# Kernel optimization log

Measured on AMD Instinct MI355X. Metric: run time of the kernel, lower is better.

The kernel has to match this reference:

```python
import jax, jax.numpy as jnp
import numpy as np

H = 2          # heads
C = 64         # hidden_dim per head
IN_DIM = 128
E_IN_DIM = 64
N_NODES = 50000
N_EDGES = 800000
NEG_SLOPE = 0.2


def gat_conv(x, edge_index, W, a_src, a_dst, bias):
    """PyG GATConv (heads=H, concat=False, add_self_loops=True).
    x: [N, F]; W: [F, H*C]; a_src/a_dst: [H, C]; bias: [C]."""
    N = x.shape[0]
    xw = (x @ W).reshape(N, H, C)                      # [N,H,C]
    loops = jnp.arange(N)
    src = jnp.concatenate([edge_index[0], loops])      # [E']
    dst = jnp.concatenate([edge_index[1], loops])
    a_s = jnp.einsum('nhc,hc->nh', xw, a_src)          # [N,H]
    a_d = jnp.einsum('nhc,hc->nh', xw, a_dst)
    e = jax.nn.leaky_relu(a_s[src] + a_d[dst], NEG_SLOPE)  # [E',H]
    # segment softmax over destination nodes (every node has a self-loop)
    m = jax.ops.segment_max(e, dst, num_segments=N)
    ex = jnp.exp(e - m[dst])
    den = jax.ops.segment_sum(ex, dst, num_segments=N)
    alpha = ex / den[dst]                              # [E',H]
    out = jax.ops.segment_sum(alpha[:, :, None] * xw[src], dst, num_segments=N)  # [N,H,C]
    return out.mean(axis=1) + bias                     # concat=False -> head mean


def setup_inputs() -> dict:
    key = jax.random.key(0)
    ks = jax.random.split(key, 16)
    s = 0.05
    return {
        'x': jax.random.normal(ks[0], (N_NODES, IN_DIM), jnp.float32),
        'xe': jax.random.normal(ks[1], (N_EDGES, E_IN_DIM), jnp.float32),
        'edge_index': jax.random.randint(ks[2], (2, N_EDGES), 0, N_NODES),
        # node GATConv params
        'Wn': jax.random.normal(ks[3], (IN_DIM, H * C), jnp.float32) * s,
        'asn': jax.random.normal(ks[4], (H, C), jnp.float32) * s,
        'adn': jax.random.normal(ks[5], (H, C), jnp.float32) * s,
        'bn': jnp.zeros((C,), jnp.float32),
        # edge GATConv params
        'We': jax.random.normal(ks[6], (E_IN_DIM, H * C), jnp.float32) * s,
        'ase': jax.random.normal(ks[7], (H, C), jnp.float32) * s,
        'ade': jax.random.normal(ks[8], (H, C), jnp.float32) * s,
        'be': jnp.zeros((C,), jnp.float32),
        # decoders
        'Wdx': jax.random.normal(ks[9], (C, IN_DIM), jnp.float32) * s,
        'bdx': jnp.zeros((IN_DIM,), jnp.float32),
        'Wde': jax.random.normal(ks[10], (C, E_IN_DIM), jnp.float32) * s,
        'bde': jnp.zeros((E_IN_DIM,), jnp.float32),
    }


def reference(x, xe, edge_index, Wn, asn, adn, bn, We, ase, ade, be, Wdx, bdx, Wde, bde):
    h_node = gat_conv(x, edge_index, Wn, asn, adn, bn)     # [N, C]
    h_edge = gat_conv(xe, edge_index, We, ase, ade, be)    # [E, C]
    x_rec = h_node @ Wdx + bdx                             # [N, in_dim]
    e_rec = h_edge @ Wde + bde                             # [E, edge_in_dim]
    return (x_rec, e_rec)
```

## Files before the change

### kernel.cpp

```cpp
#include <hip/hip_runtime.h>
#include <hip/hip_bf16.h>

constexpr int MAXD = 512;

__device__ __forceinline__ float lrelu(float v) { return v >= 0.f ? v : 0.2f * v; }

__global__ void count_kernel(const int* __restrict__ dst, int* __restrict__ cnt, int E) {
    int e = blockIdx.x * blockDim.x + threadIdx.x;
    if (e < E) atomicAdd(&cnt[dst[e]], 1);
}

__global__ __launch_bounds__(1024) void scan_kernel(const int* __restrict__ cnt, int* __restrict__ rowptr, int n) {
    __shared__ int part[1024];
    int t = threadIdx.x;
    int CH = (n + 1023) / 1024;
    int base = t * CH;
    int local = 0;
    for (int i = 0; i < CH; i++) { int idx = base + i; if (idx < n) local += cnt[idx]; }
    part[t] = local;
    __syncthreads();
    for (int o = 1; o < 1024; o <<= 1) {
        int v = (t >= o) ? part[t - o] : 0;
        __syncthreads();
        part[t] += v;
        __syncthreads();
    }
    int run = part[t] - local;
    for (int i = 0; i < CH; i++) {
        int idx = base + i;
        if (idx < n) { rowptr[idx] = run; run += cnt[idx]; }
    }
    if (t == 1023) rowptr[n] = run;
}

__global__ void scatter_kernel(const int* __restrict__ src, const int* __restrict__ dst,
                               int* __restrict__ cursor, int* __restrict__ ssrc, int E) {
    int e = blockIdx.x * blockDim.x + threadIdx.x;
    if (e < E) {
        int pos = atomicAdd(&cursor[dst[e]], 1);
        ssrc[pos] = src[e];
    }
}

__global__ void fold_kernel(const float* __restrict__ We, const float* __restrict__ Wde,
                            const float* __restrict__ be, const float* __restrict__ bde,
                            float* __restrict__ M, float* __restrict__ b0) {
    int j = threadIdx.x;
    int k = blockIdx.x;
    if (k < 64) {
        float s = 0.f;
        for (int c = 0; c < 64; c++)
            s = fmaf(0.5f * (We[k * 128 + c] + We[k * 128 + 64 + c]), Wde[c * 64 + j], s);
        M[k * 64 + j] = s;
    } else {
        float s = bde[j];
        for (int c = 0; c < 64; c++) s = fmaf(be[c], Wde[c * 64 + j], s);
        b0[j] = s;
    }
}

template <int K>
__global__ __launch_bounds__(256) void enc_gemm(const float* __restrict__ X, const float* __restrict__ W,
                                                const float* __restrict__ avs, const float* __restrict__ avd,
                                                float* __restrict__ xw, float* __restrict__ a_s,
                                                float* __restrict__ a_d, int Nn) {
    int n = blockIdx.x * 256 + threadIdx.x;
    int h = blockIdx.y;
    if (n >= Nn) return;
    const float* xr = X + (size_t)n * K;
    float acc[64];
#pragma unroll
    for (int j = 0; j < 64; j++) acc[j] = 0.f;
    for (int kc = 0; kc < K; kc += 16) {
        float xv[16];
#pragma unroll
        for (int i = 0; i < 16; i += 4) {
            float4 t = *(const float4*)(xr + kc + i);
            xv[i] = t.x; xv[i + 1] = t.y; xv[i + 2] = t.z; xv[i + 3] = t.w;
        }
#pragma unroll
        for (int k = 0; k < 16; k++) {
            const float* wr = W + (size_t)(kc + k) * 128 + h * 64;
#pragma unroll
            for (int j = 0; j < 64; j++) acc[j] = fmaf(xv[k], wr[j], acc[j]);
        }
    }
    float as = 0.f, ad = 0.f;
    const float* vs = avs + h * 64;
    const float* vd = avd + h * 64;
#pragma unroll
    for (int j = 0; j < 64; j++) { as = fmaf(acc[j], vs[j], as); ad = fmaf(acc[j], vd[j], ad); }
    float* xwr = xw + (size_t)n * 128 + h * 64;
#pragma unroll
    for (int j = 0; j < 64; j += 4) {
        float4 t = {acc[j], acc[j + 1], acc[j + 2], acc[j + 3]};
        *(float4*)(xwr + j) = t;
    }
    a_s[n * 2 + h] = as;
    a_d[n * 2 + h] = ad;
}

template <int OD>
__global__ __launch_bounds__(256) void rowmap_kernel(const float* __restrict__ A, const float* __restrict__ M,
                                                     const float* __restrict__ b0, float* __restrict__ out, int R) {
    __shared__ float4 sA4[128 * 16];
    __shared__ float4 sM4[64 * 16];
    int tid = threadIdx.x;
    int tr = tid & 15;
    int tj = tid >> 4;
    int jc = blockIdx.y * 64;
    int tile0 = blockIdx.x * 128;
    if (tile0 >= R) return;
    int nrows = min(128, R - tile0);

#pragma unroll
    for (int it = 0; it < 4; it++) {
        int f = tid + it * 256;
        int k = f >> 4, jq = f & 15;
        sM4[f] = *(const float4*)(M + (size_t)k * OD + jc + 4 * jq);
    }
    {
        const float4* Ag = (const float4*)(A + (size_t)tile0 * 64);
#pragma unroll
        for (int it = 0; it < 8; it++) {
            int e = tid + it * 256;
            int r = e >> 4, q = e & 15;
            int srcq = (r < nrows) ? e : q;
            sA4[(r << 4) | (q ^ (r & 15))] = Ag[srcq];
        }
    }
    __syncthreads();

    float4 b0v = *(const float4*)(b0 + jc + 4 * tj);
    float acc[8][4];
#pragma unroll
    for (int i = 0; i < 8; i++) { acc[i][0] = b0v.x; acc[i][1] = b0v.y; acc[i][2] = b0v.z; acc[i][3] = b0v.w; }

    for (int kq = 0; kq < 16; kq++) {
        float4 mf0 = sM4[(4 * kq + 0) * 16 + tj];
        float4 mf1 = sM4[(4 * kq + 1) * 16 + tj];
        float4 mf2 = sM4[(4 * kq + 2) * 16 + tj];
        float4 mf3 = sM4[(4 * kq + 3) * 16 + tj];
#pragma unroll
        for (int i = 0; i < 8; i++) {
            int row = tr + 16 * i;
            float4 af = sA4[(row << 4) | (kq ^ tr)];
            acc[i][0] = fmaf(af.x, mf0.x, acc[i][0]);
            acc[i][0] = fmaf(af.y, mf1.x, acc[i][0]);
            acc[i][0] = fmaf(af.z, mf2.x, acc[i][0]);
            acc[i][0] = fmaf(af.w, mf3.x, acc[i][0]);
            acc[i][1] = fmaf(af.x, mf0.y, acc[i][1]);
            acc[i][1] = fmaf(af.y, mf1.y, acc[i][1]);
            acc[i][1] = fmaf(af.z, mf2.y, acc[i][1]);
            acc[i][1] = fmaf(af.w, mf3.y, acc[i][1]);
            acc[i][2] = fmaf(af.x, mf0.z, acc[i][2]);
            acc[i][2] = fmaf(af.y, mf1.z, acc[i][2]);
            acc[i][2] = fmaf(af.z, mf2.z, acc[i][2]);
            acc[i][2] = fmaf(af.w, mf3.z, acc[i][2]);
            acc[i][3] = fmaf(af.x, mf0.w, acc[i][3]);
            acc[i][3] = fmaf(af.y, mf1.w, acc[i][3]);
            acc[i][3] = fmaf(af.z, mf2.w, acc[i][3]);
            acc[i][3] = fmaf(af.w, mf3.w, acc[i][3]);
        }
    }

#pragma unroll
    for (int i = 0; i < 8; i++) {
        int row = tr + 16 * i;
        if (row < nrows) {
            float4 t = {acc[i][0], acc[i][1], acc[i][2], acc[i][3]};
            *(float4*)(out + (size_t)(tile0 + row) * OD + jc + 4 * tj) = t;
        }
    }
}

__global__ __launch_bounds__(128) void msg_fused(
    const float* __restrict__ xw_n, const float* __restrict__ a_sn, const float* __restrict__ a_dn,
    const float* __restrict__ xw_e, const float* __restrict__ a_se, const float* __restrict__ a_de,
    const int* __restrict__ rowptr, const int* __restrict__ ssrc,
    const float* __restrict__ bn, const float* __restrict__ be,
    float* __restrict__ hm_n, float* __restrict__ hm_e) {
    int n = blockIdx.x;
    int tid = threadIdx.x;
    int h = tid >> 6, c = tid & 63;
    __shared__ int s_src[MAXD];
    __shared__ float t_n[2][MAXD];
    __shared__ float t_e[2][MAXD];
    __shared__ float red[8];
    __shared__ float hsh[2][128];

    int base = rowptr[n];
    int deg = rowptr[n + 1] - base;
    int degc = min(deg, MAXD);

    float adn0 = a_dn[n * 2 + 0], adn1 = a_dn[n * 2 + 1];
    float ade0 = a_de[n * 2 + 0], ade1 = a_de[n * 2 + 1];
    float2 asn_n = *(const float2*)(a_sn + (size_t)n * 2);
    float2 ase_n = *(const float2*)(a_se + (size_t)n * 2);
    float es_n0 = lrelu(asn_n.x + adn0), es_n1 = lrelu(asn_n.y + adn1);
    float es_e0 = lrelu(ase_n.x + ade0), es_e1 = lrelu(ase_n.y + ade1);

    for (int i = tid; i < degc; i += 128) {
        int s = ssrc[base + i];
        s_src[i] = s;
        float2 an = *(const float2*)(a_sn + (size_t)s * 2);
        float2 ae = *(const float2*)(a_se + (size_t)s * 2);
        t_n[0][i] = lrelu(an.x + adn0);
        t_n[1][i] = lrelu(an.y + adn1);
        t_e[0][i] = lrelu(ae.x + ade0);
        t_e[1][i] = lrelu(ae.y + ade1);
    }
    __syncthreads();

    int w = tid >> 6;
    int lane = tid & 63;
    {
        const float(*tt)[MAXD] = w ? t_e : t_n;
        const float* asx = w ? a_se : a_sn;
        float ad0 = w ? ade0 : adn0, ad1 = w ? ade1 : adn1;
        float es0 = w ? es_e0 : es_n0, es1 = w ? es_e1 : es_n1;
        float m0 = es0, m1 = es1;
        for (int i = lane; i < degc; i += 64) { m0 = fmaxf(m0, tt[0][i]); m1 = fmaxf(m1, tt[1][i]); }
        for (int i = MAXD + lane; i < deg; i += 64) {
            int s = ssrc[base + i];
            float2 a = *(const float2*)(asx + (size_t)s * 2);
            m0 = fmaxf(m0, lrelu(a.x + ad0)); m1 = fmaxf(m1, lrelu(a.y + ad1));
        }
#pragma unroll
        for (int o = 1; o < 64; o <<= 1) { m0 = fmaxf(m0, __shfl_xor(m0, o)); m1 = fmaxf(m1, __shfl_xor(m1, o)); }
        float d0 = 0.f, d1 = 0.f;
        for (int i = lane; i < degc; i += 64) { d0 += __expf(tt[0][i] - m0); d1 += __expf(tt[1][i] - m1); }
        for (int i = MAXD + lane; i < deg; i += 64) {
            int s = ssrc[base + i];
            float2 a = *(const float2*)(asx + (size_t)s * 2);
            d0 += __expf(lrelu(a.x + ad0) - m0); d1 += __expf(lrelu(a.y + ad1) - m1);
        }
#pragma unroll
        for (int o = 1; o < 64; o <<= 1) { d0 += __shfl_xor(d0, o); d1 += __shfl_xor(d1, o); }
        d0 += __expf(es0 - m0);
        d1 += __expf(es1 - m1);
        if (lane == 0) { red[w * 4 + 0] = m0; red[w * 4 + 1] = m1; red[w * 4 + 2] = d0; red[w * 4 + 3] = d1; }
    }
    __syncthreads();

    for (int i = tid; i < degc; i += 128) {
        t_n[0][i] = __expf(t_n[0][i] - red[0]);
        t_n[1][i] = __expf(t_n[1][i] - red[1]);
        t_e[0][i] = __expf(t_e[0][i] - red[4]);
        t_e[1][i] = __expf(t_e[1][i] - red[5]);
    }
    __syncthreads();

    float mn = red[h], dn_ = red[2 + h];
    float me = red[4 + h], de_ = red[6 + h];
    float accn = __expf((h ? es_n1 : es_n0) - mn) * xw_n[(size_t)n * 128 + h * 64 + c];
    float acce = __expf((h ? es_e1 : es_e0) - me) * xw_e[(size_t)n * 128 + h * 64 + c];
    for (int i = 0; i < degc; i++) {
        int s = s_src[i];
        float wn_ = t_n[h][i];
        float we_ = t_e[h][i];
        accn = fmaf(wn_, xw_n[(size_t)s * 128 + h * 64 + c], accn);
        acce = fmaf(we_, xw_e[(size_t)s * 128 + h * 64 + c], acce);
    }
    for (int i = MAXD; i < deg; i++) {
        int s = ssrc[base + i];
        float2 an = *(const float2*)(a_sn + (size_t)s * 2);
        float2 ae = *(const float2*)(a_se + (size_t)s * 2);
        float tn_ = lrelu(h ? (an.y + adn1) : (an.x + adn0));
        float te_ = lrelu(h ? (ae.y + ade1) : (ae.x + ade0));
        accn = fmaf(__expf(tn_ - mn), xw_n[(size_t)s * 128 + h * 64 + c], accn);
        acce = fmaf(__expf(te_ - me), xw_e[(size_t)s * 128 + h * 64 + c], acce);
    }
    hsh[0][tid] = accn / dn_;
    hsh[1][tid] = acce / de_;
    __syncthreads();
    if (tid < 64) {
        hm_n[(size_t)n * 64 + tid] = fmaf(0.5f, hsh[0][tid] + hsh[0][64 + tid], bn[tid]);
        hm_e[(size_t)n * 64 + tid] = fmaf(0.5f, hsh[1][tid] + hsh[1][64 + tid], be[tid]);
    }
}

extern "C" void kernel_launch(void* const* d_in, const int* in_sizes, int n_in,
                              void* d_out, int out_size, void* d_ws, size_t ws_size,
                              hipStream_t stream) {
    const float* x   = (const float*)d_in[0];
    const float* xe  = (const float*)d_in[1];
    const int*   ei  = (const int*)d_in[2];
    const float* Wn  = (const float*)d_in[3];
    const float* asn = (const float*)d_in[4];
    const float* adn = (const float*)d_in[5];
    const float* bn  = (const float*)d_in[6];
    const float* We  = (const float*)d_in[7];
    const float* ase = (const float*)d_in[8];
    const float* ade = (const float*)d_in[9];
    const float* be  = (const float*)d_in[10];
    const float* Wdx = (const float*)d_in[11];
    const float* bdx = (const float*)d_in[12];
    const float* Wde = (const float*)d_in[13];
    const float* bde = (const float*)d_in[14];

    const int N  = in_sizes[0] / 128;
    const int NE = in_sizes[1] / 64;
    const int E  = in_sizes[2] / 2;
    const int* src = ei;
    const int* dst = ei + E;

    char* wsb = (char*)d_ws;
    size_t off = 0;
    auto alloc = [&](size_t bytes) -> void* {
        void* p = wsb + off;
        off += (bytes + 255) & ~(size_t)255;
        return p;
    };
    float* xw_n = (float*)alloc((size_t)N * 128 * 4);
    float* a_sn = (float*)alloc((size_t)N * 2 * 4);
    float* a_dn = (float*)alloc((size_t)N * 2 * 4);
    float* xw_e = (float*)alloc((size_t)N * 128 * 4);
    float* a_se = (float*)alloc((size_t)N * 2 * 4);
    float* a_de = (float*)alloc((size_t)N * 2 * 4);
    float* hm_n = (float*)alloc((size_t)N * 64 * 4);
    float* hm_e = (float*)alloc((size_t)N * 64 * 4);
    float* Mt   = (float*)alloc((size_t)64 * 64 * 4);
    float* b0t  = (float*)alloc((size_t)64 * 4);
    int* cnt    = (int*)alloc((size_t)(N + 1) * 4);
    int* rowptr = (int*)alloc((size_t)(N + 1) * 4);
    int* cursor = (int*)alloc((size_t)(N + 1) * 4);
    int* ssrc   = (int*)alloc((size_t)E * 4);

    float* x_rec = (float*)d_out;
    float* e_rec = (float*)d_out + (size_t)N * 128;

    hipMemsetAsync(cnt, 0, (size_t)N * 4, stream);
    count_kernel<<<(E + 255) / 256, 256, 0, stream>>>(dst, cnt, E);
    scan_kernel<<<1, 1024, 0, stream>>>(cnt, rowptr, N);
    hipMemcpyAsync(cursor, rowptr, (size_t)N * 4, hipMemcpyDeviceToDevice, stream);
    scatter_kernel<<<(E + 255) / 256, 256, 0, stream>>>(src, dst, cursor, ssrc, E);

    fold_kernel<<<65, 64, 0, stream>>>(We, Wde, be, bde, Mt, b0t);

    enc_gemm<128><<<dim3((N + 255) / 256, 2), 256, 0, stream>>>(x, Wn, asn, adn, xw_n, a_sn, a_dn, N);
    enc_gemm<64><<<dim3((N + 255) / 256, 2), 256, 0, stream>>>(xe, We, ase, ade, xw_e, a_se, a_de, N);

    {
        int R = NE - N;
        rowmap_kernel<64><<<dim3((R + 127) / 128, 1), 256, 0, stream>>>(
            xe + (size_t)N * 64, Mt, b0t, e_rec + (size_t)N * 64, R);
    }

    msg_fused<<<N, 128, 0, stream>>>(xw_n, a_sn, a_dn, xw_e, a_se, a_de, rowptr, ssrc, bn, be, hm_n, hm_e);

    rowmap_kernel<128><<<dim3((N + 127) / 128, 2), 256, 0, stream>>>(hm_n, Wdx, bdx, x_rec, N);
    rowmap_kernel<64><<<dim3((N + 127) / 128, 1), 256, 0, stream>>>(hm_e, Wde, bde, e_rec, N);
}
```

Before: 846.9 us.

## Replace per-thread encoder GEMM with shared-memory tiled register-blocked GEMM

The node and edge encoder projections were computed one row per thread with 64 accumulators, reading W from global memory per FMA. They now use a 128x64 block tile staged in LDS with XOR-swizzled rows and 8x4 register blocking per thread. The attention-score dot products are reduced through shared memory. This cuts redundant global weight loads and register pressure, at the cost of extra LDS traffic and synchronisation.

```diff
diff --git a/kernel.cpp b/kernel.cpp
--- a/kernel.cpp
+++ b/kernel.cpp
@@ -60,44 +60,99 @@
 }
 
 template <int K>
-__global__ __launch_bounds__(256) void enc_gemm(const float* __restrict__ X, const float* __restrict__ W,
-                                                const float* __restrict__ avs, const float* __restrict__ avd,
-                                                float* __restrict__ xw, float* __restrict__ a_s,
-                                                float* __restrict__ a_d, int Nn) {
-    int n = blockIdx.x * 256 + threadIdx.x;
+__global__ __launch_bounds__(256) void enc_tiled(const float* __restrict__ X, const float* __restrict__ W,
+                                                 const float* __restrict__ avs, const float* __restrict__ avd,
+                                                 float* __restrict__ xw, float* __restrict__ a_s,
+                                                 float* __restrict__ a_d, int Nn) {
+    __shared__ float4 sA4[128 * 16];
+    __shared__ float4 sM4[64 * 16];
+    int tid = threadIdx.x;
+    int tr = tid & 15;
+    int tj = tid >> 4;
     int h = blockIdx.y;
-    if (n >= Nn) return;
-    const float* xr = X + (size_t)n * K;
-    float acc[64];
-#pragma unroll
-    for (int j = 0; j < 64; j++) acc[j] = 0.f;
-    for (int kc = 0; kc < K; kc += 16) {
-        float xv[16];
-#pragma unroll
-        for (int i = 0; i < 16; i += 4) {
-            float4 t = *(const float4*)(xr + kc + i);
-            xv[i] = t.x; xv[i + 1] = t.y; xv[i + 2] = t.z; xv[i + 3] = t.w;
-        }
-#pragma unroll
-        for (int k = 0; k < 16; k++) {
-            const float* wr = W + (size_t)(kc + k) * 128 + h * 64;
-#pragma unroll
-            for (int j = 0; j < 64; j++) acc[j] = fmaf(xv[k], wr[j], acc[j]);
-        }
-    }
-    float as = 0.f, ad = 0.f;
-    const float* vs = avs + h * 64;
-    const float* vd = avd + h * 64;
-#pragma unroll
-    for (int j = 0; j < 64; j++) { as = fmaf(acc[j], vs[j], as); ad = fmaf(acc[j], vd[j], ad); }
-    float* xwr = xw + (size_t)n * 128 + h * 64;
-#pragma unroll
-    for (int j = 0; j < 64; j += 4) {
-        float4 t = {acc[j], acc[j + 1], acc[j + 2], acc[j + 3]};
-        *(float4*)(xwr + j) = t;
-    }
-    a_s[n * 2 + h] = as;
-    a_d[n * 2 + h] = ad;
+    int jc = h * 64;
+    int tile0 = blockIdx.x * 128;
+    if (tile0 >= Nn) return;
+    int nrows = min(128, Nn - tile0);
+
+    float acc[8][4];
+#pragma unroll
+    for (int i = 0; i < 8; i++) { acc[i][0] = 0.f; acc[i][1] = 0.f; acc[i][2] = 0.f; acc[i][3] = 0.f; }
+
+    for (int kc = 0; kc < K; kc += 64) {
+        if (kc) __syncthreads();
+#pragma unroll
+        for (int it = 0; it < 4; it++) {
+            int f = tid + it * 256;
+            int k = f >> 4, jq = f & 15;
+            sM4[f] = *(const float4*)(W + (size_t)(kc + k) * 128 + jc + 4 * jq);
+        }
+#pragma unroll
+        for (int it = 0; it < 8; it++) {
+            int e = tid + it * 256;
+            int r = e >> 4, q = e & 15;
+            int rs = (r < nrows) ? r : 0;
+            sA4[(r << 4) | (q ^ (r & 15))] = *(const float4*)(X + (size_t)(tile0 + rs) * K + kc + 4 * q);
+        }
+        __syncthreads();
+        for (int kq = 0; kq < 16; kq++) {
+            float4 mf0 = sM4[(4 * kq + 0) * 16 + tj];
+            float4 mf1 = sM4[(4 * kq + 1) * 16 + tj];
+            float4 mf2 = sM4[(4 * kq + 2) * 16 + tj];
+            float4 mf3 = sM4[(4 * kq + 3) * 16 + tj];
+#pragma unroll
+            for (int i = 0; i < 8; i++) {
+                int row = tr + 16 * i;
+                float4 af = sA4[(row << 4) | (kq ^ tr)];
+                acc[i][0] = fmaf(af.x, mf0.x, acc[i][0]);
+                acc[i][0] = fmaf(af.y, mf1.x, acc[i][0]);
+                acc[i][0] = fmaf(af.z, mf2.x, acc[i][0]);
+                acc[i][0] = fmaf(af.w, mf3.x, acc[i][0]);
+                acc[i][1] = fmaf(af.x, mf0.y, acc[i][1]);
+                acc[i][1] = fmaf(af.y, mf1.y, acc[i][1]);
+                acc[i][1] = fmaf(af.z, mf2.y, acc[i][1]);
+                acc[i][1] = fmaf(af.w, mf3.y, acc[i][1]);
+                acc[i][2] = fmaf(af.x, mf0.z, acc[i][2]);
+                acc[i][2] = fmaf(af.y, mf1.z, acc[i][2]);
+                acc[i][2] = fmaf(af.z, mf2.z, acc[i][2]);
+                acc[i][2] = fmaf(af.w, mf3.z, acc[i][2]);
+                acc[i][3] = fmaf(af.x, mf0.w, acc[i][3]);
+                acc[i][3] = fmaf(af.y, mf1.w, acc[i][3]);
+                acc[i][3] = fmaf(af.z, mf2.w, acc[i][3]);
+                acc[i][3] = fmaf(af.w, mf3.w, acc[i][3]);
+            }
+        }
+    }
+
+#pragma unroll
+    for (int i = 0; i < 8; i++) {
+        int row = tr + 16 * i;
+        if (row < nrows) {
+            float4 t = {acc[i][0], acc[i][1], acc[i][2], acc[i][3]};
+            *(float4*)(xw + (size_t)(tile0 + row) * 128 + jc + 4 * tj) = t;
+        }
+    }
+
+    float4 vs = *(const float4*)(avs + jc + 4 * tj);
+    float4 vd = *(const float4*)(avd + jc + 4 * tj);
+    __syncthreads();
+    float* red = (float*)sA4;
+#pragma unroll
+    for (int i = 0; i < 8; i++) {
+        int row = tr + 16 * i;
+        float ps = acc[i][0] * vs.x + acc[i][1] * vs.y + acc[i][2] * vs.z + acc[i][3] * vs.w;
+        float pd = acc[i][0] * vd.x + acc[i][1] * vd.y + acc[i][2] * vd.z + acc[i][3] * vd.w;
+        red[row * 17 + tj] = ps;
+        red[4096 + row * 17 + tj] = pd;
+    }
+    __syncthreads();
+    if (tid < 128 && tid < nrows) {
+        float ss = 0.f, sd = 0.f;
+#pragma unroll
+        for (int t = 0; t < 16; t++) { ss += red[tid * 17 + t]; sd += red[4096 + tid * 17 + t]; }
+        a_s[(size_t)(tile0 + tid) * 2 + h] = ss;
+        a_d[(size_t)(tile0 + tid) * 2 + h] = sd;
+    }
 }
 
 template <int OD>
@@ -338,8 +393,8 @@
 
     fold_kernel<<<65, 64, 0, stream>>>(We, Wde, be, bde, Mt, b0t);
 
-    enc_gemm<128><<<dim3((N + 255) / 256, 2), 256, 0, stream>>>(x, Wn, asn, adn, xw_n, a_sn, a_dn, N);
-    enc_gemm<64><<<dim3((N + 255) / 256, 2), 256, 0, stream>>>(xe, We, ase, ade, xw_e, a_se, a_de, N);
+    enc_tiled<128><<<dim3((N + 127) / 128, 2), 256, 0, stream>>>(x, Wn, asn, adn, xw_n, a_sn, a_dn, N);
+    enc_tiled<64><<<dim3((N + 127) / 128, 2), 256, 0, stream>>>(xe, We, ase, ade, xw_e, a_se, a_de, N);
 
     {
         int R = NE - N;
```

Result: faster. 791.1 us (-6.6%).
